# Kernel optimization log

Measured on AMD Instinct MI355X. Metric: run time of the kernel, lower is better.

The kernel has to match this reference:

```python
import jax, jax.numpy as jnp
import numpy as np

_CODESZ = 8

def _cartesian8(vals):
    # matches torch.cartesian_prod ordering ('ij' meshgrid)
    grids = np.meshgrid(*([vals] * _CODESZ), indexing='ij')
    return np.stack(grids, axis=-1).reshape(-1, _CODESZ)

def _build_grid():
    intr = np.arange(-2, 2, dtype=np.float32)
    hintr = intr + 0.5
    ge8 = np.concatenate([_cartesian8(intr), _cartesian8(hintr)], axis=0)
    m2 = (ge8.sum(axis=-1) % 2) == 0
    nrm = (ge8 ** 2).sum(axis=-1) <= 3
    e8 = ge8[m2 & nrm]
    extra = np.array([
        [1,1,1,0,0,1,0,0],[1,1,0,0,1,1,0,0],[1,0,0,1,1,1,0,0],[0,0,1,1,1,1,0,0],
        [0,1,1,1,0,1,0,0],[1,1,1,0,0,0,1,0],[1,1,0,0,1,0,1,0],[1,0,0,1,1,0,1,0],
        [0,0,1,1,1,0,1,0],[0,1,1,1,0,0,1,0],[1,1,1,0,0,0,0,1],[1,1,0,0,1,0,0,1],
        [1,0,0,1,1,0,0,1],[0,0,1,1,1,0,0,1],[0,1,1,1,0,0,0,1]], dtype=np.float32)
    return np.concatenate([e8, extra], axis=0)  # [256, 8]

def setup_inputs() -> dict:
    key = jax.random.key(0)
    N = 1048576
    X = jax.random.normal(key, (N, _CODESZ), dtype=jnp.float32)
    grid_np = _build_grid()
    grid = jnp.asarray(grid_np)                       # [256, 8]
    grid_norm = jnp.asarray((grid_np ** 2).sum(-1))   # [256]
    return {"X": X, "grid": grid, "grid_norm": grid_norm}

def reference(X, grid, grid_norm):
    scores = 2.0 * jnp.einsum('nd,cd->nc', X, grid) - grid_norm  # [N, 256]
    idx = jnp.argmax(scores, axis=-1)                            # [N]
    Xq = grid[idx]                                               # [N, 8]
    return Xq, idx.astype(jnp.uint8)
```

## Files before the change

### kernel.cpp

```cpp
#include <hip/hip_runtime.h>
#include <stdint.h>


#define DIM 8
#define NCODES 256

struct Tables {
    unsigned char pair_idx[256];
    unsigned char half_idx[256];
    unsigned char zero_idx;
};

constexpr Tables make_tables() {
    Tables t{};
    unsigned key[113] = {};
    int pi[113] = {}, pj[113] = {}, psi[113] = {}, psj[113] = {};
    int n = 0;
    {
        unsigned k = 0;
        for (int d = 0; d < 8; ++d) k = k * 4u + 2u;
        key[n] = k; pi[n] = -1; pj[n] = -1; psi[n] = 0; psj[n] = 0; ++n;
    }
    for (int i = 0; i < 8; ++i)
        for (int j = i + 1; j < 8; ++j)
            for (int a = 0; a < 2; ++a)
                for (int b = 0; b < 2; ++b) {
                    unsigned k = 0;
                    for (int d = 0; d < 8; ++d) {
                        unsigned dig = 2u;
                        if (d == i) dig = a ? 1u : 3u;
                        if (d == j) dig = b ? 1u : 3u;
                        k = k * 4u + dig;
                    }
                    key[n] = k; pi[n] = i; pj[n] = j; psi[n] = a; psj[n] = b; ++n;
                }
    for (int p = 1; p < n; ++p) {
        unsigned kk = key[p]; int a = pi[p], b = pj[p], c = psi[p], d2 = psj[p];
        int q = p - 1;
        while (q >= 0 && key[q] > kk) {
            key[q+1]=key[q]; pi[q+1]=pi[q]; pj[q+1]=pj[q]; psi[q+1]=psi[q]; psj[q+1]=psj[q]; --q;
        }
        key[q+1]=kk; pi[q+1]=a; pj[q+1]=b; psi[q+1]=c; psj[q+1]=d2;
    }
    for (int r = 0; r < n; ++r) {
        if (pi[r] < 0) t.zero_idx = (unsigned char)r;
        else t.pair_idx[(((pi[r]*8 + pj[r])*2 + psi[r])*2) + psj[r]] = (unsigned char)r;
    }
    unsigned hkey[128] = {}; int hm[128] = {}; int hn = 0;
    for (int m = 0; m < 256; ++m) {
        int pc = 0; for (int d = 0; d < 8; ++d) pc += (m >> d) & 1;
        if (pc & 1) continue;
        unsigned k = 0;
        for (int d = 0; d < 8; ++d) k = k * 4u + (((m >> d) & 1) ? 1u : 2u);
        hkey[hn] = k; hm[hn] = m; ++hn;
    }
    for (int p = 1; p < hn; ++p) {
        unsigned kk = hkey[p]; int mm = hm[p]; int q = p - 1;
        while (q >= 0 && hkey[q] > kk) { hkey[q+1]=hkey[q]; hm[q+1]=hm[q]; --q; }
        hkey[q+1]=kk; hm[q+1]=mm;
    }
    for (int r = 0; r < hn; ++r) t.half_idx[hm[r]] = (unsigned char)(113 + r);
    return t;
}

constexpr Tables h_tab = make_tables();
__constant__ Tables g_tab = h_tab;

template <int MODE>
__global__ __launch_bounds__(256)
void e8_decode_kernel(const float* __restrict__ X,
                      const float* __restrict__ grid,
                      const float* __restrict__ gnorm,
                      float* __restrict__ xq_out,
                      void* __restrict__ idx_out,
                      int N)
{
    const long pt = (long)blockIdx.x * blockDim.x + threadIdx.x;
    if (pt >= N) return;
    const int lane = threadIdx.x & 63;

    const float4* xsrc = reinterpret_cast<const float4*>(X + pt * DIM);
    const float4 xa = xsrc[0];
    const float4 xb = xsrc[1];
    float x[8] = {xa.x, xa.y, xa.z, xa.w, xb.x, xb.y, xb.z, xb.w};

    float a[8]; uint32_t sb[8];
    #pragma unroll
    for (int d = 0; d < 8; ++d) {
        const uint32_t u = __float_as_uint(x[d]);
        sb[d] = u >> 31;
        a[d] = __uint_as_float(u & 0x7fffffffu);
    }
    uint32_t mask = 0, par = 0;
    #pragma unroll
    for (int d = 0; d < 8; ++d) { mask |= sb[d] << d; par ^= sb[d]; }
    const bool odd = (par != 0);

    float S = a[0];
    #pragma unroll
    for (int d = 1; d < 8; ++d) S += a[d];

    float mn = a[0]; int mi = 0;
    #pragma unroll
    for (int d = 1; d < 8; ++d) { const bool lt = a[d] < mn; mn = lt ? a[d] : mn; mi = lt ? d : mi; }
    float mn2 = 3.0e38f;
    #pragma unroll
    for (int d = 0; d < 8; ++d) { const float v = (d == mi) ? 3.0e38f : a[d]; mn2 = fminf(mn2, v); }

    float m1 = a[0]; int i1 = 0;
    #pragma unroll
    for (int d = 1; d < 8; ++d) { const bool gt = a[d] > m1; m1 = gt ? a[d] : m1; i1 = gt ? d : i1; }
    float m2 = -3.0e38f; int i2 = 0;
    #pragma unroll
    for (int d = 0; d < 8; ++d) {
        const float v = (d == i1) ? -3.0e38f : a[d];
        const bool gt = v > m2; m2 = gt ? v : m2; i2 = gt ? d : i2;
    }
    float m3 = -3.0e38f;
    #pragma unroll
    for (int d = 0; d < 8; ++d) {
        const float v = (d == i1 || d == i2) ? -3.0e38f : a[d];
        m3 = fmaxf(m3, v);
    }

    const float s_pair = fmaf(2.0f, m1 + m2, -2.0f);
    const float s_half = odd ? (fmaf(-2.0f, mn, S) - 2.0f) : (S - 2.0f);

    const float y01 = x[0] + x[1];
    float b[5];
    b[0] = y01 + x[2];
    b[1] = y01 + x[4];
    b[2] = (x[0] + x[3]) + x[4];
    b[3] = (x[2] + x[3]) + x[4];
    b[4] = (x[1] + x[2]) + x[3];
    float bm = b[0]; int bi = 0;
    #pragma unroll
    for (int k = 1; k < 5; ++k) { const bool gt = b[k] > bm; bm = gt ? b[k] : bm; bi = gt ? k : bi; }
    float b2nd = -3.0e38f;
    #pragma unroll
    for (int k = 0; k < 5; ++k) { const float v = (k == bi) ? -3.0e38f : b[k]; b2nd = fmaxf(b2nd, v); }
    float tm = x[5]; int ti = 0;
    { const bool gt = x[6] > tm; tm = gt ? x[6] : tm; ti = gt ? 1 : ti; }
    { const bool gt = x[7] > tm; tm = gt ? x[7] : tm; ti = gt ? 2 : ti; }
    const float t2 = fmaxf(fminf(fmaxf(x[5], x[6]), x[7]), fminf(x[5], x[6]));
    const float s_extra = fmaf(2.0f, bm + tm, -4.0f);

    const float r_pair  = fmaf(2.0f, m1 + m3, -2.0f);
    const float r_half  = odd ? (fmaf(-2.0f, mn2, S) - 2.0f)
                              : (fmaf(-2.0f, mn + mn2, S) - 2.0f);
    const float r_extra = fmaf(2.0f, fmaxf(b2nd + tm, bm + t2), -4.0f);

    const int lo = (i1 < i2) ? i1 : i2;
    const int hi = (i1 < i2) ? i2 : i1;
    const uint32_t slo = (mask >> lo) & 1u;
    const uint32_t shi = (mask >> hi) & 1u;
    const int idx_pair  = g_tab.pair_idx[(((lo << 3) + hi) << 2) + (int)((slo << 1) | shi)];
    const uint32_t hmask = odd ? (mask ^ (1u << mi)) : mask;
    const int idx_half  = g_tab.half_idx[hmask & 255u];
    const int idx_extra = 241 + ti * 5 + bi;
    const int idx_zero  = g_tab.zero_idx;

    float best = s_pair; int bidx = idx_pair; float sec = -3.0e38f;
    {
        const float s = 0.0f; const int id = idx_zero;
        const bool gt = s > best;
        const bool take = gt || (s == best && id < bidx);
        sec = fmaxf(sec, gt ? best : s);
        best = gt ? s : best;
        bidx = take ? id : bidx;
    }
    {
        const float s = s_half; const int id = idx_half;
        const bool gt = s > best;
        const bool take = gt || (s == best && id < bidx);
        sec = fmaxf(sec, gt ? best : s);
        best = gt ? s : best;
        bidx = take ? id : bidx;
    }
    {
        const float s = s_extra; const int id = idx_extra;
        const bool gt = s > best;
        const bool take = gt || (s == best && id < bidx);
        sec = fmaxf(sec, gt ? best : s);
        best = gt ? s : best;
        bidx = take ? id : bidx;
    }
    sec = fmaxf(fmaxf(sec, r_pair), fmaxf(r_half, r_extra));

    const bool fb = !((best - sec) > 6.4e-5f) || !(mn > 0.0f);
    uint64_t bal = __ballot(fb);
    while (bal) {
        const int src = __ffsll((unsigned long long)bal) - 1;
        bal &= bal - 1;
        float xs[8];
        #pragma unroll
        for (int d = 0; d < 8; ++d) xs[d] = __shfl(x[d], src);
        float2 xv[4];
        #pragma unroll
        for (int q = 0; q < 4; ++q)
            xv[q] = make_float2(2.0f * xs[2*q], 2.0f * xs[2*q + 1]);
        float bb = -3.4e38f; int bbi = 0;
        #pragma unroll
        for (int u = 0; u < 4; ++u) {
            const int c = (lane << 2) + u;
            const float2* g2 = reinterpret_cast<const float2*>(grid + c * DIM);
            float2 acc = xv[0] * g2[0];
            acc += xv[1] * g2[1];
            acc += xv[2] * g2[2];
            acc += xv[3] * g2[3];
            const float s = (acc.x + acc.y) - gnorm[c];
            const bool gt = s > bb;
            bb = gt ? s : bb; bbi = gt ? c : bbi;
        }
        #pragma unroll
        for (int off = 32; off >= 1; off >>= 1) {
            const float so = __shfl_xor(bb, off);
            const int   io = __shfl_xor(bbi, off);
            const bool take = (so > bb) || (so == bb && io < bbi);
            bb  = take ? so : bb;
            bbi = take ? io : bbi;
        }
        if (lane == src) bidx = bbi;
    }

    const float4* gr = reinterpret_cast<const float4*>(grid + (long)bidx * DIM);
    const float4 q0 = gr[0];
    const float4 q1 = gr[1];
    float4* dst = reinterpret_cast<float4*>(xq_out + pt * DIM);
    dst[0] = q0;
    dst[1] = q1;
    if (MODE == 2) {
        reinterpret_cast<float*>(idx_out)[pt] = (float)bidx;
    } else if (MODE == 1) {
        reinterpret_cast<uint8_t*>(idx_out)[pt] = (uint8_t)bidx;
    }
}

extern "C" void kernel_launch(void* const* d_in, const int* in_sizes, int n_in,
                              void* d_out, int out_size, void* d_ws, size_t ws_size,
                              hipStream_t stream)
{
    const float* X     = (const float*)d_in[0];
    const float* grid  = (const float*)d_in[1];
    const float* gnorm = (const float*)d_in[2];

    const int N = in_sizes[0] / DIM;

    float* xq   = (float*)d_out;
    void*  idxp = (void*)(xq + (size_t)N * DIM);

    const int blocks = (N + 255) / 256;

    const long xq_elems = (long)N * DIM;
    if ((long)out_size >= xq_elems + N) {
        e8_decode_kernel<2><<<blocks, 256, 0, stream>>>(X, grid, gnorm, xq, idxp, N);
    } else if ((long)out_size > xq_elems) {
        e8_decode_kernel<1><<<blocks, 256, 0, stream>>>(X, grid, gnorm, xq, idxp, N);
    } else {
        e8_decode_kernel<0><<<blocks, 256, 0, stream>>>(X, grid, gnorm, xq, idxp, N);
    }
}
```

Before: 89.05 us.

## Process four points per thread and synthesize codewords from bits instead of grid gather

Each thread now handles four points, with their loads issued up front to raise memory-level parallelism. In the common fast path the output codeword is built directly from sign and support bitmasks, so the per-point grid gather is skipped. The grid is only read when the fallback brute-force search ran. Launch bounds now request higher occupancy. The trade-offs are more registers per thread and a per-class bit-construction path that has to match the grid layout exactly.

```diff
diff --git a/kernel.cpp b/kernel.cpp
--- a/kernel.cpp
+++ b/kernel.cpp
@@ -4,6 +4,7 @@
 
 #define DIM 8
 #define NCODES 256
+#define PPT 4
 
 struct Tables {
     unsigned char pair_idx[256];
@@ -67,7 +68,7 @@
 __constant__ Tables g_tab = h_tab;
 
 template <int MODE>
-__global__ __launch_bounds__(256)
+__global__ __launch_bounds__(256, 4)
 void e8_decode_kernel(const float* __restrict__ X,
                       const float* __restrict__ grid,
                       const float* __restrict__ gnorm,
@@ -75,164 +76,208 @@
                       void* __restrict__ idx_out,
                       int N)
 {
-    const long pt = (long)blockIdx.x * blockDim.x + threadIdx.x;
-    if (pt >= N) return;
-    const int lane = threadIdx.x & 63;
-
-    const float4* xsrc = reinterpret_cast<const float4*>(X + pt * DIM);
-    const float4 xa = xsrc[0];
-    const float4 xb = xsrc[1];
-    float x[8] = {xa.x, xa.y, xa.z, xa.w, xb.x, xb.y, xb.z, xb.w};
-
-    float a[8]; uint32_t sb[8];
+    const int lane  = threadIdx.x & 63;
+    const int gw    = (int)((blockIdx.x * blockDim.x + threadIdx.x) >> 6);
+    const int wbase = gw * (64 * PPT);
+
+    float4 xa[PPT], xb[PPT];
     #pragma unroll
-    for (int d = 0; d < 8; ++d) {
-        const uint32_t u = __float_as_uint(x[d]);
-        sb[d] = u >> 31;
-        a[d] = __uint_as_float(u & 0x7fffffffu);
-    }
-    uint32_t mask = 0, par = 0;
+    for (int p = 0; p < PPT; ++p) {
+        const int pt = wbase + p * 64 + lane;
+        xa[p] = make_float4(0.f, 0.f, 0.f, 0.f);
+        xb[p] = xa[p];
+        if (pt < N) {
+            const float4* s = reinterpret_cast<const float4*>(X + (size_t)pt * DIM);
+            xa[p] = s[0];
+            xb[p] = s[1];
+        }
+    }
+
     #pragma unroll
-    for (int d = 0; d < 8; ++d) { mask |= sb[d] << d; par ^= sb[d]; }
-    const bool odd = (par != 0);
-
-    float S = a[0];
-    #pragma unroll
-    for (int d = 1; d < 8; ++d) S += a[d];
-
-    float mn = a[0]; int mi = 0;
-    #pragma unroll
-    for (int d = 1; d < 8; ++d) { const bool lt = a[d] < mn; mn = lt ? a[d] : mn; mi = lt ? d : mi; }
-    float mn2 = 3.0e38f;
-    #pragma unroll
-    for (int d = 0; d < 8; ++d) { const float v = (d == mi) ? 3.0e38f : a[d]; mn2 = fminf(mn2, v); }
-
-    float m1 = a[0]; int i1 = 0;
-    #pragma unroll
-    for (int d = 1; d < 8; ++d) { const bool gt = a[d] > m1; m1 = gt ? a[d] : m1; i1 = gt ? d : i1; }
-    float m2 = -3.0e38f; int i2 = 0;
-    #pragma unroll
-    for (int d = 0; d < 8; ++d) {
-        const float v = (d == i1) ? -3.0e38f : a[d];
-        const bool gt = v > m2; m2 = gt ? v : m2; i2 = gt ? d : i2;
-    }
-    float m3 = -3.0e38f;
-    #pragma unroll
-    for (int d = 0; d < 8; ++d) {
-        const float v = (d == i1 || d == i2) ? -3.0e38f : a[d];
-        m3 = fmaxf(m3, v);
-    }
-
-    const float s_pair = fmaf(2.0f, m1 + m2, -2.0f);
-    const float s_half = odd ? (fmaf(-2.0f, mn, S) - 2.0f) : (S - 2.0f);
-
-    const float y01 = x[0] + x[1];
-    float b[5];
-    b[0] = y01 + x[2];
-    b[1] = y01 + x[4];
-    b[2] = (x[0] + x[3]) + x[4];
-    b[3] = (x[2] + x[3]) + x[4];
-    b[4] = (x[1] + x[2]) + x[3];
-    float bm = b[0]; int bi = 0;
-    #pragma unroll
-    for (int k = 1; k < 5; ++k) { const bool gt = b[k] > bm; bm = gt ? b[k] : bm; bi = gt ? k : bi; }
-    float b2nd = -3.0e38f;
-    #pragma unroll
-    for (int k = 0; k < 5; ++k) { const float v = (k == bi) ? -3.0e38f : b[k]; b2nd = fmaxf(b2nd, v); }
-    float tm = x[5]; int ti = 0;
-    { const bool gt = x[6] > tm; tm = gt ? x[6] : tm; ti = gt ? 1 : ti; }
-    { const bool gt = x[7] > tm; tm = gt ? x[7] : tm; ti = gt ? 2 : ti; }
-    const float t2 = fmaxf(fminf(fmaxf(x[5], x[6]), x[7]), fminf(x[5], x[6]));
-    const float s_extra = fmaf(2.0f, bm + tm, -4.0f);
-
-    const float r_pair  = fmaf(2.0f, m1 + m3, -2.0f);
-    const float r_half  = odd ? (fmaf(-2.0f, mn2, S) - 2.0f)
-                              : (fmaf(-2.0f, mn + mn2, S) - 2.0f);
-    const float r_extra = fmaf(2.0f, fmaxf(b2nd + tm, bm + t2), -4.0f);
-
-    const int lo = (i1 < i2) ? i1 : i2;
-    const int hi = (i1 < i2) ? i2 : i1;
-    const uint32_t slo = (mask >> lo) & 1u;
-    const uint32_t shi = (mask >> hi) & 1u;
-    const int idx_pair  = g_tab.pair_idx[(((lo << 3) + hi) << 2) + (int)((slo << 1) | shi)];
-    const uint32_t hmask = odd ? (mask ^ (1u << mi)) : mask;
-    const int idx_half  = g_tab.half_idx[hmask & 255u];
-    const int idx_extra = 241 + ti * 5 + bi;
-    const int idx_zero  = g_tab.zero_idx;
-
-    float best = s_pair; int bidx = idx_pair; float sec = -3.0e38f;
-    {
-        const float s = 0.0f; const int id = idx_zero;
-        const bool gt = s > best;
-        const bool take = gt || (s == best && id < bidx);
-        sec = fmaxf(sec, gt ? best : s);
-        best = gt ? s : best;
-        bidx = take ? id : bidx;
-    }
-    {
-        const float s = s_half; const int id = idx_half;
-        const bool gt = s > best;
-        const bool take = gt || (s == best && id < bidx);
-        sec = fmaxf(sec, gt ? best : s);
-        best = gt ? s : best;
-        bidx = take ? id : bidx;
-    }
-    {
-        const float s = s_extra; const int id = idx_extra;
-        const bool gt = s > best;
-        const bool take = gt || (s == best && id < bidx);
-        sec = fmaxf(sec, gt ? best : s);
-        best = gt ? s : best;
-        bidx = take ? id : bidx;
-    }
-    sec = fmaxf(fmaxf(sec, r_pair), fmaxf(r_half, r_extra));
-
-    const bool fb = !((best - sec) > 6.4e-5f) || !(mn > 0.0f);
-    uint64_t bal = __ballot(fb);
-    while (bal) {
-        const int src = __ffsll((unsigned long long)bal) - 1;
-        bal &= bal - 1;
-        float xs[8];
-        #pragma unroll
-        for (int d = 0; d < 8; ++d) xs[d] = __shfl(x[d], src);
-        float2 xv[4];
-        #pragma unroll
-        for (int q = 0; q < 4; ++q)
-            xv[q] = make_float2(2.0f * xs[2*q], 2.0f * xs[2*q + 1]);
-        float bb = -3.4e38f; int bbi = 0;
-        #pragma unroll
-        for (int u = 0; u < 4; ++u) {
-            const int c = (lane << 2) + u;
-            const float2* g2 = reinterpret_cast<const float2*>(grid + c * DIM);
-            float2 acc = xv[0] * g2[0];
-            acc += xv[1] * g2[1];
-            acc += xv[2] * g2[2];
-            acc += xv[3] * g2[3];
-            const float s = (acc.x + acc.y) - gnorm[c];
-            const bool gt = s > bb;
-            bb = gt ? s : bb; bbi = gt ? c : bbi;
-        }
-        #pragma unroll
-        for (int off = 32; off >= 1; off >>= 1) {
-            const float so = __shfl_xor(bb, off);
-            const int   io = __shfl_xor(bbi, off);
-            const bool take = (so > bb) || (so == bb && io < bbi);
-            bb  = take ? so : bb;
-            bbi = take ? io : bbi;
-        }
-        if (lane == src) bidx = bbi;
-    }
-
-    const float4* gr = reinterpret_cast<const float4*>(grid + (long)bidx * DIM);
-    const float4 q0 = gr[0];
-    const float4 q1 = gr[1];
-    float4* dst = reinterpret_cast<float4*>(xq_out + pt * DIM);
-    dst[0] = q0;
-    dst[1] = q1;
-    if (MODE == 2) {
-        reinterpret_cast<float*>(idx_out)[pt] = (float)bidx;
-    } else if (MODE == 1) {
-        reinterpret_cast<uint8_t*>(idx_out)[pt] = (uint8_t)bidx;
+    for (int p = 0; p < PPT; ++p) {
+        const int pt = wbase + p * 64 + lane;
+        const bool valid = pt < N;
+        float x[8] = {xa[p].x, xa[p].y, xa[p].z, xa[p].w,
+                      xb[p].x, xb[p].y, xb[p].z, xb[p].w};
+
+        float a[8]; uint32_t sb[8];
+        #pragma unroll
+        for (int d = 0; d < 8; ++d) {
+            const uint32_t u = __float_as_uint(x[d]);
+            sb[d] = u >> 31;
+            a[d] = __uint_as_float(u & 0x7fffffffu);
+        }
+        uint32_t mask = 0, par = 0;
+        #pragma unroll
+        for (int d = 0; d < 8; ++d) { mask |= sb[d] << d; par ^= sb[d]; }
+        const bool odd = (par != 0);
+
+        float S = a[0];
+        #pragma unroll
+        for (int d = 1; d < 8; ++d) S += a[d];
+
+        float mn = a[0]; int mi = 0;
+        #pragma unroll
+        for (int d = 1; d < 8; ++d) { const bool lt = a[d] < mn; mn = lt ? a[d] : mn; mi = lt ? d : mi; }
+        float mn2 = 3.0e38f;
+        #pragma unroll
+        for (int d = 0; d < 8; ++d) { const float v = (d == mi) ? 3.0e38f : a[d]; mn2 = fminf(mn2, v); }
+
+        float m1 = a[0]; int i1 = 0;
+        #pragma unroll
+        for (int d = 1; d < 8; ++d) { const bool gt = a[d] > m1; m1 = gt ? a[d] : m1; i1 = gt ? d : i1; }
+        float m2 = -3.0e38f; int i2 = 0;
+        #pragma unroll
+        for (int d = 0; d < 8; ++d) {
+            const float v = (d == i1) ? -3.0e38f : a[d];
+            const bool gt = v > m2; m2 = gt ? v : m2; i2 = gt ? d : i2;
+        }
+        float m3 = -3.0e38f;
+        #pragma unroll
+        for (int d = 0; d < 8; ++d) {
+            const float v = (d == i1 || d == i2) ? -3.0e38f : a[d];
+            m3 = fmaxf(m3, v);
+        }
+
+        const float s_pair = fmaf(2.0f, m1 + m2, -2.0f);
+        const float s_half = odd ? (fmaf(-2.0f, mn, S) - 2.0f) : (S - 2.0f);
+
+        const float y01 = x[0] + x[1];
+        float b[5];
+        b[0] = y01 + x[2];
+        b[1] = y01 + x[4];
+        b[2] = (x[0] + x[3]) + x[4];
+        b[3] = (x[2] + x[3]) + x[4];
+        b[4] = (x[1] + x[2]) + x[3];
+        float bm = b[0]; int bi = 0;
+        #pragma unroll
+        for (int k = 1; k < 5; ++k) { const bool gt = b[k] > bm; bm = gt ? b[k] : bm; bi = gt ? k : bi; }
+        float b2nd = -3.0e38f;
+        #pragma unroll
+        for (int k = 0; k < 5; ++k) { const float v = (k == bi) ? -3.0e38f : b[k]; b2nd = fmaxf(b2nd, v); }
+        float tm = x[5]; int ti = 0;
+        { const bool gt = x[6] > tm; tm = gt ? x[6] : tm; ti = gt ? 1 : ti; }
+        { const bool gt = x[7] > tm; tm = gt ? x[7] : tm; ti = gt ? 2 : ti; }
+        const float t2 = fmaxf(fminf(fmaxf(x[5], x[6]), x[7]), fminf(x[5], x[6]));
+        const float s_extra = fmaf(2.0f, bm + tm, -4.0f);
+
+        const float r_pair  = fmaf(2.0f, m1 + m3, -2.0f);
+        const float r_half  = odd ? (fmaf(-2.0f, mn2, S) - 2.0f)
+                                  : (fmaf(-2.0f, mn + mn2, S) - 2.0f);
+        const float r_extra = fmaf(2.0f, fmaxf(b2nd + tm, bm + t2), -4.0f);
+
+        const int lo = (i1 < i2) ? i1 : i2;
+        const int hi = (i1 < i2) ? i2 : i1;
+        const uint32_t slo = (mask >> lo) & 1u;
+        const uint32_t shi = (mask >> hi) & 1u;
+        const int idx_pair  = g_tab.pair_idx[(((lo << 3) + hi) << 2) + (int)((slo << 1) | shi)];
+        const uint32_t hmask = odd ? (mask ^ (1u << mi)) : mask;
+        const int idx_half  = g_tab.half_idx[hmask & 255u];
+        const int idx_extra = 241 + ti * 5 + bi;
+        const int idx_zero  = g_tab.zero_idx;
+        const uint32_t emask = (uint32_t)((0x0E1C191307ULL >> (bi * 8)) & 0xFFu)
+                             | (1u << (5 + ti));
+
+        float best = s_pair; int bidx = idx_pair; int cls = 0; float sec = -3.0e38f;
+        {
+            const float s = 0.0f; const int id = idx_zero;
+            const bool gt = s > best;
+            const bool take = gt || (s == best && id < bidx);
+            sec = fmaxf(sec, gt ? best : s);
+            best = gt ? s : best;
+            bidx = take ? id : bidx;
+            cls  = take ? 1 : cls;
+        }
+        {
+            const float s = s_half; const int id = idx_half;
+            const bool gt = s > best;
+            const bool take = gt || (s == best && id < bidx);
+            sec = fmaxf(sec, gt ? best : s);
+            best = gt ? s : best;
+            bidx = take ? id : bidx;
+            cls  = take ? 2 : cls;
+        }
+        {
+            const float s = s_extra; const int id = idx_extra;
+            const bool gt = s > best;
+            const bool take = gt || (s == best && id < bidx);
+            sec = fmaxf(sec, gt ? best : s);
+            best = gt ? s : best;
+            bidx = take ? id : bidx;
+            cls  = take ? 3 : cls;
+        }
+        sec = fmaxf(fmaxf(sec, r_pair), fmaxf(r_half, r_extra));
+
+        const bool fb = (!((best - sec) > 6.4e-5f) || !(mn > 0.0f)) && valid;
+        uint64_t bal = __ballot(fb);
+        while (bal) {
+            const int src = __ffsll((unsigned long long)bal) - 1;
+            bal &= bal - 1;
+            float xs[8];
+            #pragma unroll
+            for (int d = 0; d < 8; ++d) xs[d] = __shfl(x[d], src);
+            float2 xv[4];
+            #pragma unroll
+            for (int q = 0; q < 4; ++q)
+                xv[q] = make_float2(2.0f * xs[2*q], 2.0f * xs[2*q + 1]);
+            float bb = -3.4e38f; int bbi = 0;
+            #pragma unroll
+            for (int u = 0; u < 4; ++u) {
+                const int c = (lane << 2) + u;
+                const float2* g2 = reinterpret_cast<const float2*>(grid + c * DIM);
+                float2 acc = xv[0] * g2[0];
+                acc += xv[1] * g2[1];
+                acc += xv[2] * g2[2];
+                acc += xv[3] * g2[3];
+                const float s = (acc.x + acc.y) - gnorm[c];
+                const bool gt = s > bb;
+                bb = gt ? s : bb; bbi = gt ? c : bbi;
+            }
+            #pragma unroll
+            for (int off = 32; off >= 1; off >>= 1) {
+                const float so = __shfl_xor(bb, off);
+                const int   io = __shfl_xor(bbi, off);
+                const bool take = (so > bb) || (so == bb && io < bbi);
+                bb  = take ? so : bb;
+                bbi = take ? io : bbi;
+            }
+            if (lane == src) bidx = bbi;
+        }
+
+        uint32_t M    = (1u << lo) | (1u << hi);
+        uint32_t base = 0x3F800000u;
+        uint32_t smask = mask;
+        if (cls == 1) { M = 0u; }
+        if (cls == 2) { M = 0xFFu; base = 0x3F000000u; smask = hmask; }
+        if (cls == 3) { M = emask; base = 0x3F800000u; smask = 0u; }
+
+        uint32_t bits[8];
+        #pragma unroll
+        for (int d = 0; d < 8; ++d) {
+            const uint32_t mb = (M >> d) & 1u;
+            const uint32_t sg = ((smask >> d) & 1u) << 31;
+            bits[d] = mb ? (base | sg) : 0u;
+        }
+        float4 q0 = make_float4(__uint_as_float(bits[0]), __uint_as_float(bits[1]),
+                                __uint_as_float(bits[2]), __uint_as_float(bits[3]));
+        float4 q1 = make_float4(__uint_as_float(bits[4]), __uint_as_float(bits[5]),
+                                __uint_as_float(bits[6]), __uint_as_float(bits[7]));
+        if (fb) {
+            const float4* gr = reinterpret_cast<const float4*>(grid + (size_t)bidx * DIM);
+            q0 = gr[0];
+            q1 = gr[1];
+        }
+
+        if (valid) {
+            float4* dst = reinterpret_cast<float4*>(xq_out + (size_t)pt * DIM);
+            dst[0] = q0;
+            dst[1] = q1;
+            if (MODE == 2) {
+                reinterpret_cast<float*>(idx_out)[pt] = (float)bidx;
+            } else if (MODE == 1) {
+                reinterpret_cast<uint8_t*>(idx_out)[pt] = (uint8_t)bidx;
+            }
+        }
     }
 }
 
@@ -249,7 +294,8 @@
     float* xq   = (float*)d_out;
     void*  idxp = (void*)(xq + (size_t)N * DIM);
 
-    const int blocks = (N + 255) / 256;
+    const int threads = (N + PPT - 1) / PPT;
+    const int blocks  = (threads + 255) / 256;
 
     const long xq_elems = (long)N * DIM;
     if ((long)out_size >= xq_elems + N) {
```

After: 92.98 us. 4.4% more time.
